# Performance work log

Hardware: AMD Instinct MI355X
Metric: run time of the kernel (lower is better)

Reference implementation:

```python
import jax, jax.numpy as jnp
import numpy as np

N_NODES = 100000
N_EDGES = 3200000
DROP_P = 0.5  # F.dropout default, training=True


def gcn_conv(x, row, col, ew, W, b, n):
    # PyG GCNConv with add_self_loops=True, normalize=True:
    # A_hat = A + I, deg = sum of edge weights at target, out = D^-1/2 A_hat D^-1/2 (x W) + b
    loop = jnp.arange(n, dtype=row.dtype)
    r = jnp.concatenate([row, loop])
    c = jnp.concatenate([col, loop])
    w = jnp.concatenate([ew, jnp.ones((n,), dtype=ew.dtype)])
    deg = jax.ops.segment_sum(w, c, num_segments=n)
    dis = jnp.where(deg > 0, jax.lax.rsqrt(deg), 0.0)
    norm = dis[r] * w * dis[c]                      # [E+N]
    h = x @ W                                        # [N, D_out]
    msg = norm[:, None] * h[r]                       # [E+N, D_out]
    out = jax.ops.segment_sum(msg, c, num_segments=n)
    return out + b


def dropout(x, key, p=DROP_P):
    keep = jax.random.bernoulli(key, 1.0 - p, x.shape)
    return jnp.where(keep, x / (1.0 - p), 0.0)


def setup_inputs() -> dict:
    key = jax.random.key(0)
    ks = jax.random.split(key, 9)
    node_features = jax.random.normal(ks[0], (N_NODES, 128), dtype=jnp.float32)
    edge_index = jax.random.randint(ks[1], (2, N_EDGES), 0, N_NODES, dtype=jnp.int64)
    edge_weight = jax.random.uniform(ks[2], (N_EDGES,), dtype=jnp.float32)
    W1 = jax.random.normal(ks[3], (128, 128), dtype=jnp.float32) * 0.05
    b1 = jnp.zeros((128,), dtype=jnp.float32)
    W2 = jax.random.normal(ks[4], (128, 128), dtype=jnp.float32) * 0.05
    b2 = jnp.zeros((128,), dtype=jnp.float32)
    W3 = jax.random.normal(ks[5], (128, 64), dtype=jnp.float32) * 0.05
    b3 = jnp.zeros((64,), dtype=jnp.float32)
    return dict(node_features=node_features, edge_index=edge_index, edge_weight=edge_weight,
                W1=W1, b1=b1, W2=W2, b2=b2, W3=W3, b3=b3)


def reference(node_features, edge_index, edge_weight, W1, b1, W2, b2, W3, b3):
    n = node_features.shape[0]
    row, col = edge_index[0], edge_index[1]
    dk1, dk2 = jax.random.split(jax.random.key(42))
    x = gcn_conv(node_features, row, col, edge_weight, W1, b1, n)
    x = dropout(jax.nn.relu(x), dk1)
    x = gcn_conv(x, row, col, edge_weight, W2, b2, n)
    x = dropout(jax.nn.relu(x), dk2)
    x = gcn_conv(x, row, col, edge_weight, W3, b3, n)
    return x
```

## Files before the change

kernel.cpp:

```cpp
#include <hip/hip_runtime.h>
#include <hip/hip_bf16.h>
#include <hip/hip_fp16.h>
#include <stdint.h>

typedef unsigned int u32;

__host__ __device__ constexpr void tf_block(u32 k0, u32 k1, u32& x0, u32& x1) {
  const u32 ks2 = k0 ^ k1 ^ 0x1BD11BDAu;
  const u32 ks[3] = {k0, k1, ks2};
  const int R[2][4] = {{13, 15, 26, 6}, {17, 29, 16, 24}};
  x0 += k0;
  x1 += k1;
  for (int i = 0; i < 5; ++i) {
    for (int j = 0; j < 4; ++j) {
      const int r = R[i & 1][j];
      x0 += x1;
      x1 = (x1 << r) | (x1 >> (32 - r));
      x1 ^= x0;
    }
    x0 += ks[(i + 1) % 3];
    x1 += ks[(i + 2) % 3] + (u32)(i + 1);
  }
}

struct KeyPair { u32 a, b; };
__host__ __device__ constexpr KeyPair tf_pair(u32 k0, u32 k1, u32 c0, u32 c1) {
  u32 x0 = c0, x1 = c1;
  tf_block(k0, k1, x0, x1);
  return KeyPair{x0, x1};
}

constexpr KeyPair DK1 = tf_pair(0u, 42u, 0u, 0u);
constexpr KeyPair DK2 = tf_pair(0u, 42u, 0u, 1u);

__device__ __forceinline__ bool keep_elem(u32 ka, u32 kb, u32 idx) {
  u32 x0 = 0u, x1 = idx;
  tf_block(ka, kb, x0, x1);
  return ((x0 ^ x1) & 0x80000000u) == 0u;
}

__global__ void detect_kernel(const u32* __restrict__ ei, u32* __restrict__ flag) {
  if (threadIdx.x == 0) {
    u32 acc = 0;
    for (int k = 0; k < 32; ++k) acc |= ei[2 * k + 1];
    *flag = (acc == 0u) ? 1u : 0u;
  }
}

__global__ void zero_counts(u32* __restrict__ b, int n) {
  const int i = blockIdx.x * blockDim.x + threadIdx.x;
  if (i < n) b[i] = 0u;
}

__global__ __launch_bounds__(256) void edge_count(
    const u32* __restrict__ ei, u32* __restrict__ counts, int E,
    const u32* __restrict__ flag) {
  const int e = blockIdx.x * 256 + threadIdx.x;
  if (e >= E) return;
  const bool is64 = (*flag != 0u);
  const u32 c = is64 ? ei[2 * ((size_t)E + e)] : ei[(size_t)E + e];
  atomicAdd(&counts[c], 1u);
}

__global__ __launch_bounds__(1024) void scan_kernel(
    const u32* __restrict__ counts, u32* __restrict__ offsets,
    u32* __restrict__ cursor, int N) {
  __shared__ u32 wsum[16];
  __shared__ u32 carry_s;
  const int t = threadIdx.x, lane = t & 63, wv = t >> 6;
  if (t == 0) carry_s = 0u;
  __syncthreads();
  for (int base = 0; base < N; base += 1024) {
    const int i = base + t;
    const u32 v = (i < N) ? counts[i] : 0u;
    u32 inc = v;
#pragma unroll
    for (int off = 1; off < 64; off <<= 1) {
      const u32 tmp = (u32)__shfl_up((int)inc, off, 64);
      if (lane >= off) inc += tmp;
    }
    if (lane == 63) wsum[wv] = inc;
    __syncthreads();
    if (wv == 0) {
      u32 wval = (lane < 16) ? wsum[lane] : 0u;
#pragma unroll
      for (int off = 1; off < 16; off <<= 1) {
        const u32 tmp = (u32)__shfl_up((int)wval, off, 64);
        if (lane >= off) wval += tmp;
      }
      if (lane < 16) wsum[lane] = wval;
    }
    __syncthreads();
    const u32 c0 = carry_s;
    const u32 wpre = (wv == 0) ? 0u : wsum[wv - 1];
    const u32 excl = c0 + wpre + inc - v;
    if (i < N) { offsets[i] = excl; cursor[i] = excl; }
    __syncthreads();
    if (t == 0) carry_s = c0 + wsum[15];
    __syncthreads();
  }
  if (t == 0) offsets[N] = carry_s;
}

__global__ __launch_bounds__(256) void scatter_kernel(
    const u32* __restrict__ ei, const float* __restrict__ ew,
    u32* __restrict__ cursor, uint2* __restrict__ srcw, int E,
    const u32* __restrict__ flag) {
  const int e = blockIdx.x * 256 + threadIdx.x;
  if (e >= E) return;
  const bool is64 = (*flag != 0u);
  u32 r, c;
  if (is64) { r = ei[2 * (size_t)e]; c = ei[2 * ((size_t)E + e)]; }
  else      { r = ei[e];             c = ei[(size_t)E + e]; }
  const u32 pos = atomicAdd(&cursor[c], 1u);
  srcw[pos] = make_uint2(r, __float_as_uint(ew[e]));
}

__global__ __launch_bounds__(256) void degsum_kernel(
    const uint2* __restrict__ srcw, const u32* __restrict__ offsets,
    float* __restrict__ dis, int N) {
  const int lane = threadIdx.x & 63;
  const int wid = blockIdx.x * 4 + (threadIdx.x >> 6);
  if (wid >= N) return;
  const u32 beg = offsets[wid], end = offsets[wid + 1];
  float a = 0.f;
  for (u32 e = beg + lane; e < end; e += 64)
    a += __uint_as_float(srcw[e].y);
#pragma unroll
  for (int off = 32; off > 0; off >>= 1)
    a += __shfl_xor(a, off, 64);
  if (lane == 0) dis[wid] = rsqrtf(a + 1.0f);
}

template <int DOUT>
__global__ __launch_bounds__(256) void gemm_scale(
    const float* __restrict__ x, const float* __restrict__ W,
    const float* __restrict__ dis, __half* __restrict__ hs, int N) {
  static_assert(DOUT == 128 || DOUT == 64, "");
  constexpr int ROWS = 64;
  constexpr int CT = DOUT / 32;
  constexpr int RT = 8;
  __shared__ float wlds[128 * DOUT];
  __shared__ float xlds[ROWS * 128];

  const int tid = threadIdx.x;
  const int rowbase = blockIdx.x * ROWS;

  for (int i = tid * 4; i < 128 * DOUT; i += 256 * 4)
    *(float4*)(wlds + i) = *(const float4*)(W + i);
  for (int i = tid * 4; i < ROWS * 128; i += 256 * 4) {
    const int r = i >> 7, k = i & 127;
    const int row = rowbase + r;
    float4 v = make_float4(0.f, 0.f, 0.f, 0.f);
    if (row < N) v = *(const float4*)(x + (size_t)row * 128 + k);
    *(float4*)(xlds + i) = v;
  }
  __syncthreads();

  const int c0 = tid & 31;
  const int rg = tid >> 5;
  float acc[RT][CT];
#pragma unroll
  for (int r = 0; r < RT; ++r)
#pragma unroll
    for (int cc = 0; cc < CT; ++cc) acc[r][cc] = 0.f;

  for (int k = 0; k < 128; k += 4) {
    float4 xv[RT];
#pragma unroll
    for (int r = 0; r < RT; ++r)
      xv[r] = *(const float4*)(xlds + (rg * RT + r) * 128 + k);
#pragma unroll
    for (int kk = 0; kk < 4; ++kk) {
      float wv[CT];
#pragma unroll
      for (int cc = 0; cc < CT; ++cc)
        wv[cc] = wlds[(k + kk) * DOUT + c0 + 32 * cc];
#pragma unroll
      for (int r = 0; r < RT; ++r) {
        const float xk = (kk == 0) ? xv[r].x : (kk == 1) ? xv[r].y
                        : (kk == 2) ? xv[r].z : xv[r].w;
#pragma unroll
        for (int cc = 0; cc < CT; ++cc)
          acc[r][cc] = fmaf(xk, wv[cc], acc[r][cc]);
      }
    }
  }

#pragma unroll
  for (int r = 0; r < RT; ++r) {
    const int row = rowbase + rg * RT + r;
    if (row >= N) continue;
    const float d = dis[row];
#pragma unroll
    for (int cc = 0; cc < CT; ++cc)
      hs[(size_t)row * DOUT + c0 + 32 * cc] = __float2half(d * acc[r][cc]);
  }
}

template <int DOUT, bool ACT>
__global__ __launch_bounds__(256) void aggregate_k(
    const uint2* __restrict__ srcw, const u32* __restrict__ offsets,
    const float* __restrict__ dis, const __half* __restrict__ hs,
    const float* __restrict__ bias, float* __restrict__ out, int N,
    u32 ka, u32 kb) {
  const int lane = threadIdx.x & 63;
  const int wid = blockIdx.x * 4 + (threadIdx.x >> 6);
  if (wid >= N) return;
  const u32 beg = offsets[wid], end = offsets[wid + 1];

  if constexpr (DOUT == 128) {
    const int f0 = lane * 2;
    float ax = 0.f, ay = 0.f;
    u32 e = beg;
    for (; e + 4 <= end; e += 4) {
      const uint2 s0 = srcw[e + 0], s1 = srcw[e + 1], s2 = srcw[e + 2], s3 = srcw[e + 3];
      const __half2 h0 = *(const __half2*)(hs + (size_t)s0.x * 128 + f0);
      const __half2 h1 = *(const __half2*)(hs + (size_t)s1.x * 128 + f0);
      const __half2 h2 = *(const __half2*)(hs + (size_t)s2.x * 128 + f0);
      const __half2 h3 = *(const __half2*)(hs + (size_t)s3.x * 128 + f0);
      const float2 v0 = __half22float2(h0);
      const float2 v1 = __half22float2(h1);
      const float2 v2 = __half22float2(h2);
      const float2 v3 = __half22float2(h3);
      const float w0 = __uint_as_float(s0.y), w1 = __uint_as_float(s1.y);
      const float w2 = __uint_as_float(s2.y), w3 = __uint_as_float(s3.y);
      ax = fmaf(w0, v0.x, ax); ay = fmaf(w0, v0.y, ay);
      ax = fmaf(w1, v1.x, ax); ay = fmaf(w1, v1.y, ay);
      ax = fmaf(w2, v2.x, ax); ay = fmaf(w2, v2.y, ay);
      ax = fmaf(w3, v3.x, ax); ay = fmaf(w3, v3.y, ay);
    }
    for (; e < end; ++e) {
      const uint2 s0 = srcw[e];
      const float2 v0 = __half22float2(*(const __half2*)(hs + (size_t)s0.x * 128 + f0));
      const float w0 = __uint_as_float(s0.y);
      ax = fmaf(w0, v0.x, ax); ay = fmaf(w0, v0.y, ay);
    }
    const float d = dis[wid];
    const float2 sv = __half22float2(*(const __half2*)(hs + (size_t)wid * 128 + f0));
    float ox = d * (ax + sv.x) + bias[f0];
    float oy = d * (ay + sv.y) + bias[f0 + 1];
    if constexpr (ACT) {
      ox = fmaxf(ox, 0.f);
      oy = fmaxf(oy, 0.f);
      const u32 idx = (u32)wid * 128u + (u32)f0;
      ox = keep_elem(ka, kb, idx) ? 2.f * ox : 0.f;
      oy = keep_elem(ka, kb, idx + 1u) ? 2.f * oy : 0.f;
    }
    *(float2*)(out + (size_t)wid * 128 + f0) = make_float2(ox, oy);
  } else {
    float a = 0.f;
    u32 e = beg;
    for (; e + 4 <= end; e += 4) {
      const uint2 s0 = srcw[e + 0], s1 = srcw[e + 1], s2 = srcw[e + 2], s3 = srcw[e + 3];
      const float v0 = __half2float(hs[(size_t)s0.x * 64 + lane]);
      const float v1 = __half2float(hs[(size_t)s1.x * 64 + lane]);
      const float v2 = __half2float(hs[(size_t)s2.x * 64 + lane]);
      const float v3 = __half2float(hs[(size_t)s3.x * 64 + lane]);
      a = fmaf(__uint_as_float(s0.y), v0, a);
      a = fmaf(__uint_as_float(s1.y), v1, a);
      a = fmaf(__uint_as_float(s2.y), v2, a);
      a = fmaf(__uint_as_float(s3.y), v3, a);
    }
    for (; e < end; ++e) {
      const uint2 s0 = srcw[e];
      a = fmaf(__uint_as_float(s0.y), __half2float(hs[(size_t)s0.x * 64 + lane]), a);
    }
    const float d = dis[wid];
    const float o = d * (a + __half2float(hs[(size_t)wid * 64 + lane])) + bias[lane];
    out[(size_t)wid * 64 + lane] = o;
  }
}

extern "C" void kernel_launch(void* const* d_in, const int* in_sizes, int n_in,
                              void* d_out, int out_size, void* d_ws, size_t ws_size,
                              hipStream_t stream) {
  const float* x0 = (const float*)d_in[0];
  const u32* ei   = (const u32*)d_in[1];
  const float* ew = (const float*)d_in[2];
  const float* W1 = (const float*)d_in[3];
  const float* b1 = (const float*)d_in[4];
  const float* W2 = (const float*)d_in[5];
  const float* b2 = (const float*)d_in[6];
  const float* W3 = (const float*)d_in[7];
  const float* b3 = (const float*)d_in[8];

  const int N = in_sizes[0] / 128;
  const int E = in_sizes[2];

  char* p = (char*)d_ws;
  auto carve = [&](size_t bytes) -> char* {
    char* q = p;
    p += (bytes + 255) & ~(size_t)255;
    return q;
  };
  u32*    counts = (u32*)carve((size_t)N * 4);
  u32*    offs   = (u32*)carve((size_t)(N + 1) * 4);
  u32*    cursor = (u32*)carve((size_t)N * 4);
  float*  dis    = (float*)carve((size_t)N * 4);
  u32*    flag   = (u32*)carve(256);
  uint2*  srcw   = (uint2*)carve((size_t)E * 8);
  __half* hs     = (__half*)carve((size_t)N * 128 * 2);
  float*  xbuf   = (float*)carve((size_t)N * 128 * 4);

  const int egrid = (E + 255) / 256;
  const int ngrid = (N + 255) / 256;
  const int ggrid = (N + 63) / 64;
  const int agrid = (N + 3) / 4;

  detect_kernel<<<1, 64, 0, stream>>>(ei, flag);
  zero_counts<<<ngrid, 256, 0, stream>>>(counts, N);
  edge_count<<<egrid, 256, 0, stream>>>(ei, counts, E, flag);
  scan_kernel<<<1, 1024, 0, stream>>>(counts, offs, cursor, N);
  scatter_kernel<<<egrid, 256, 0, stream>>>(ei, ew, cursor, srcw, E, flag);
  degsum_kernel<<<agrid, 256, 0, stream>>>(srcw, offs, dis, N);

  gemm_scale<128><<<ggrid, 256, 0, stream>>>(x0, W1, dis, hs, N);
  aggregate_k<128, true><<<agrid, 256, 0, stream>>>(srcw, offs, dis, hs, b1, xbuf, N, DK1.a, DK1.b);
  gemm_scale<128><<<ggrid, 256, 0, stream>>>(xbuf, W2, dis, hs, N);
  aggregate_k<128, true><<<agrid, 256, 0, stream>>>(srcw, offs, dis, hs, b2, xbuf, N, DK2.a, DK2.b);
  gemm_scale<64><<<ggrid, 256, 0, stream>>>(xbuf, W3, dis, hs, N);
  aggregate_k<64, false><<<agrid, 256, 0, stream>>>(srcw, offs, dis, hs, b3, (float*)d_out, N, 0u, 0u);
}
```

Baseline: 1.174 ms.

## Replace global-atomic CSR build with two-level bucket sort using LDS atomics

Builds the destination-sorted edge list in two passes. First 128 chunk blocks histogram edges into 128-node buckets in LDS, then a scan produces per-(bucket,chunk) offsets and edges are scattered into buckets with LDS cursors. A per-bucket sort then places edges by node, which also fuses the degree sum and rsqrt. This replaces millions of contended global atomics and the separate degree pass, at the cost of an extra pass over the edges, only 128 blocks in the count and scatter phases, and a 20-bit source-index packing limit.

```diff
diff --git a/kernel.cpp b/kernel.cpp
--- a/kernel.cpp
+++ b/kernel.cpp
@@ -4,6 +4,8 @@
 #include <stdint.h>
 
 typedef unsigned int u32;
+
+constexpr int NB = 128;
 
 __host__ __device__ constexpr void tf_block(u32 k0, u32 k1, u32& x0, u32& x1) {
   const u32 ks2 = k0 ^ k1 ^ 0x1BD11BDAu;
@@ -47,32 +49,36 @@
   }
 }
 
-__global__ void zero_counts(u32* __restrict__ b, int n) {
-  const int i = blockIdx.x * blockDim.x + threadIdx.x;
-  if (i < n) b[i] = 0u;
-}
-
-__global__ __launch_bounds__(256) void edge_count(
-    const u32* __restrict__ ei, u32* __restrict__ counts, int E,
-    const u32* __restrict__ flag) {
-  const int e = blockIdx.x * 256 + threadIdx.x;
-  if (e >= E) return;
+__global__ __launch_bounds__(256) void partA_count(
+    const u32* __restrict__ ei, u32* __restrict__ part_hist,
+    int E, int P, int CHUNK, const u32* __restrict__ flag) {
+  extern __shared__ u32 lhist[];
+  const int blk = blockIdx.x;
+  for (int i = threadIdx.x; i < P; i += 256) lhist[i] = 0u;
+  __syncthreads();
   const bool is64 = (*flag != 0u);
-  const u32 c = is64 ? ei[2 * ((size_t)E + e)] : ei[(size_t)E + e];
-  atomicAdd(&counts[c], 1u);
+  const int lo = blk * CHUNK;
+  const int hi = min(lo + CHUNK, E);
+  for (int e = lo + threadIdx.x; e < hi; e += 256) {
+    const u32 c = is64 ? ei[2 * ((size_t)E + e)] : ei[(size_t)E + e];
+    atomicAdd(&lhist[c >> 7], 1u);
+  }
+  __syncthreads();
+  for (int b = threadIdx.x; b < P; b += 256)
+    part_hist[(size_t)b * NB + blk] = lhist[b];
 }
 
 __global__ __launch_bounds__(1024) void scan_kernel(
-    const u32* __restrict__ counts, u32* __restrict__ offsets,
-    u32* __restrict__ cursor, int N) {
+    const u32* __restrict__ in, u32* __restrict__ out, int L,
+    u32* __restrict__ node_offs, int N, int E) {
   __shared__ u32 wsum[16];
   __shared__ u32 carry_s;
   const int t = threadIdx.x, lane = t & 63, wv = t >> 6;
   if (t == 0) carry_s = 0u;
   __syncthreads();
-  for (int base = 0; base < N; base += 1024) {
+  for (int base = 0; base < L; base += 1024) {
     const int i = base + t;
-    const u32 v = (i < N) ? counts[i] : 0u;
+    const u32 v = (i < L) ? in[i] : 0u;
     u32 inc = v;
 #pragma unroll
     for (int off = 1; off < 64; off <<= 1) {
@@ -94,42 +100,79 @@
     const u32 c0 = carry_s;
     const u32 wpre = (wv == 0) ? 0u : wsum[wv - 1];
     const u32 excl = c0 + wpre + inc - v;
-    if (i < N) { offsets[i] = excl; cursor[i] = excl; }
+    if (i < L) out[i] = excl;
     __syncthreads();
     if (t == 0) carry_s = c0 + wsum[15];
     __syncthreads();
   }
-  if (t == 0) offsets[N] = carry_s;
-}
-
-__global__ __launch_bounds__(256) void scatter_kernel(
+  if (t == 0) {
+    out[L] = carry_s;
+    node_offs[N] = (u32)E;
+  }
+}
+
+__global__ __launch_bounds__(256) void partC_scatter(
     const u32* __restrict__ ei, const float* __restrict__ ew,
-    u32* __restrict__ cursor, uint2* __restrict__ srcw, int E,
-    const u32* __restrict__ flag) {
-  const int e = blockIdx.x * 256 + threadIdx.x;
-  if (e >= E) return;
+    const u32* __restrict__ scanned, uint2* __restrict__ part,
+    int E, int P, int CHUNK, const u32* __restrict__ flag) {
+  extern __shared__ u32 lcur[];
+  const int blk = blockIdx.x;
+  for (int b = threadIdx.x; b < P; b += 256)
+    lcur[b] = scanned[(size_t)b * NB + blk];
+  __syncthreads();
   const bool is64 = (*flag != 0u);
-  u32 r, c;
-  if (is64) { r = ei[2 * (size_t)e]; c = ei[2 * ((size_t)E + e)]; }
-  else      { r = ei[e];             c = ei[(size_t)E + e]; }
-  const u32 pos = atomicAdd(&cursor[c], 1u);
-  srcw[pos] = make_uint2(r, __float_as_uint(ew[e]));
-}
-
-__global__ __launch_bounds__(256) void degsum_kernel(
-    const uint2* __restrict__ srcw, const u32* __restrict__ offsets,
-    float* __restrict__ dis, int N) {
-  const int lane = threadIdx.x & 63;
-  const int wid = blockIdx.x * 4 + (threadIdx.x >> 6);
-  if (wid >= N) return;
-  const u32 beg = offsets[wid], end = offsets[wid + 1];
-  float a = 0.f;
-  for (u32 e = beg + lane; e < end; e += 64)
-    a += __uint_as_float(srcw[e].y);
-#pragma unroll
-  for (int off = 32; off > 0; off >>= 1)
-    a += __shfl_xor(a, off, 64);
-  if (lane == 0) dis[wid] = rsqrtf(a + 1.0f);
+  const int lo = blk * CHUNK;
+  const int hi = min(lo + CHUNK, E);
+  for (int e = lo + threadIdx.x; e < hi; e += 256) {
+    u32 r, c;
+    if (is64) { r = ei[2 * (size_t)e]; c = ei[2 * ((size_t)E + e)]; }
+    else      { r = ei[e];             c = ei[(size_t)E + e]; }
+    const u32 pos = atomicAdd(&lcur[c >> 7], 1u);
+    part[pos] = make_uint2(r | ((c & 127u) << 20), __float_as_uint(ew[e]));
+  }
+}
+
+__global__ __launch_bounds__(256) void bucket_sort(
+    const uint2* __restrict__ part, const u32* __restrict__ scanned,
+    u32* __restrict__ node_offs, float* __restrict__ dis,
+    uint2* __restrict__ srcw, int N) {
+  __shared__ u32 cnt[128];
+  __shared__ float wsum[128];
+  __shared__ u32 excl[128];
+  const int b = blockIdx.x;
+  const int t = threadIdx.x;
+  const u32 beg = scanned[(size_t)b * NB];
+  const u32 end = scanned[(size_t)(b + 1) * NB];
+  if (t < 128) { cnt[t] = 0u; wsum[t] = 0.f; }
+  __syncthreads();
+  for (u32 e = beg + t; e < end; e += 256) {
+    const uint2 it = part[e];
+    const u32 nl = it.x >> 20;
+    atomicAdd(&cnt[nl], 1u);
+    atomicAdd(&wsum[nl], __uint_as_float(it.y));
+  }
+  __syncthreads();
+  if (t == 0) {
+    u32 s = 0;
+    for (int i = 0; i < 128; ++i) { excl[i] = s; s += cnt[i]; }
+  }
+  __syncthreads();
+  const int node0 = b << 7;
+  if (t < 128) {
+    const int node = node0 + t;
+    if (node < N) {
+      node_offs[node] = beg + excl[t];
+      dis[node] = rsqrtf(wsum[t] + 1.0f);
+    }
+    cnt[t] = excl[t];
+  }
+  __syncthreads();
+  for (u32 e = beg + t; e < end; e += 256) {
+    const uint2 it = part[e];
+    const u32 nl = it.x >> 20;
+    const u32 pos = beg + atomicAdd(&cnt[nl], 1u);
+    srcw[pos] = make_uint2(it.x & 0xFFFFFu, it.y);
+  }
 }
 
 template <int DOUT>
@@ -287,6 +330,9 @@
 
   const int N = in_sizes[0] / 128;
   const int E = in_sizes[2];
+  const int P = (N + 127) >> 7;
+  const int L = P * NB;
+  const int CHUNK = (E + NB - 1) / NB;
 
   char* p = (char*)d_ws;
   auto carve = [&](size_t bytes) -> char* {
@@ -294,31 +340,30 @@
     p += (bytes + 255) & ~(size_t)255;
     return q;
   };
-  u32*    counts = (u32*)carve((size_t)N * 4);
-  u32*    offs   = (u32*)carve((size_t)(N + 1) * 4);
-  u32*    cursor = (u32*)carve((size_t)N * 4);
-  float*  dis    = (float*)carve((size_t)N * 4);
-  u32*    flag   = (u32*)carve(256);
-  uint2*  srcw   = (uint2*)carve((size_t)E * 8);
-  __half* hs     = (__half*)carve((size_t)N * 128 * 2);
-  float*  xbuf   = (float*)carve((size_t)N * 128 * 4);
-
-  const int egrid = (E + 255) / 256;
-  const int ngrid = (N + 255) / 256;
+  u32*    part_hist = (u32*)carve((size_t)L * 4);
+  u32*    scanned   = (u32*)carve((size_t)(L + 1) * 4);
+  u32*    node_offs = (u32*)carve((size_t)(N + 1) * 4);
+  float*  dis       = (float*)carve((size_t)N * 4);
+  u32*    flag      = (u32*)carve(256);
+  uint2*  srcw      = (uint2*)carve((size_t)E * 8);
+  __half* hs        = (__half*)carve((size_t)N * 128 * 2);
+  float*  xbuf      = (float*)carve((size_t)N * 128 * 4);
+  uint2*  part      = (uint2*)xbuf;
+
   const int ggrid = (N + 63) / 64;
   const int agrid = (N + 3) / 4;
+  const size_t lds_p = (size_t)P * 4;
 
   detect_kernel<<<1, 64, 0, stream>>>(ei, flag);
-  zero_counts<<<ngrid, 256, 0, stream>>>(counts, N);
-  edge_count<<<egrid, 256, 0, stream>>>(ei, counts, E, flag);
-  scan_kernel<<<1, 1024, 0, stream>>>(counts, offs, cursor, N);
-  scatter_kernel<<<egrid, 256, 0, stream>>>(ei, ew, cursor, srcw, E, flag);
-  degsum_kernel<<<agrid, 256, 0, stream>>>(srcw, offs, dis, N);
+  partA_count<<<NB, 256, lds_p, stream>>>(ei, part_hist, E, P, CHUNK, flag);
+  scan_kernel<<<1, 1024, 0, stream>>>(part_hist, scanned, L, node_offs, N, E);
+  partC_scatter<<<NB, 256, lds_p, stream>>>(ei, ew, scanned, part, E, P, CHUNK, flag);
+  bucket_sort<<<P, 256, 0, stream>>>(part, scanned, node_offs, dis, srcw, N);
 
   gemm_scale<128><<<ggrid, 256, 0, stream>>>(x0, W1, dis, hs, N);
-  aggregate_k<128, true><<<agrid, 256, 0, stream>>>(srcw, offs, dis, hs, b1, xbuf, N, DK1.a, DK1.b);
+  aggregate_k<128, true><<<agrid, 256, 0, stream>>>(srcw, node_offs, dis, hs, b1, xbuf, N, DK1.a, DK1.b);
   gemm_scale<128><<<ggrid, 256, 0, stream>>>(xbuf, W2, dis, hs, N);
-  aggregate_k<128, true><<<agrid, 256, 0, stream>>>(srcw, offs, dis, hs, b2, xbuf, N, DK2.a, DK2.b);
+  aggregate_k<128, true><<<agrid, 256, 0, stream>>>(srcw, node_offs, dis, hs, b2, xbuf, N, DK2.a, DK2.b);
   gemm_scale<64><<<ggrid, 256, 0, stream>>>(xbuf, W3, dis, hs, N);
-  aggregate_k<64, false><<<agrid, 256, 0, stream>>>(srcw, offs, dis, hs, b3, (float*)d_out, N, 0u, 0u);
-}
+  aggregate_k<64, false><<<agrid, 256, 0, stream>>>(srcw, node_offs, dis, hs, b3, (float*)d_out, N, 0u, 0u);
+}
```

Measured after the change: 1.060 ms. 9.7% less time.
